# Optimization experiments

Hardware: AMD Instinct MI355X
Metric: run time of the kernel (lower is better)

## Reference

```python
import jax, jax.numpy as jnp
import numpy as np

N = 50000      # nodes
E = 500000     # directed edges
F_IN = 112     # node feature dim
G = 256        # number of graphs in batch


def _lin(key, fan_in, fan_out):
    # torch nn.Linear default init: U(-1/sqrt(fan_in), 1/sqrt(fan_in))
    s = 1.0 / np.sqrt(fan_in)
    kw, kb = jax.random.split(key)
    W = jax.random.uniform(kw, (fan_in, fan_out), jnp.float32, -s, s)
    b = jax.random.uniform(kb, (fan_out,), jnp.float32, -s, s)
    return W, b


def setup_inputs() -> dict:
    key = jax.random.key(0)
    ks = jax.random.split(key, 9)
    x = jax.random.normal(ks[0], (N, F_IN), jnp.float32)
    edge_index = jax.random.randint(ks[1], (2, E), 0, N)
    # sorted graph ids, guaranteeing every graph id 0..G-1 appears
    batch = jnp.sort(jnp.concatenate([jnp.arange(G),
                                      jax.random.randint(ks[2], (N - G,), 0, G)]))
    W1, b1 = _lin(ks[3], F_IN, 336)
    W2, b2 = _lin(ks[4], 336, 168)
    Wg, bg = _lin(ks[5], 168, 84)
    Wf, bf = _lin(ks[6], 84, 42)
    Wo, bo = _lin(ks[7], 42, 1)
    return dict(x=x, edge_index=edge_index, batch=batch,
                W1=W1, b1=b1, W2=W2, b2=b2,
                Wg=Wg, bg=bg, Wf=Wf, bf=bf, Wo=Wo, bo=bo)


def _gcn_conv(x, W, b, src, dst, n):
    """PyG GCNConv: add self-loops, symmetric D^-1/2 A D^-1/2 normalization."""
    h = x @ W                                   # [n, out]
    loop = jnp.arange(n, dtype=src.dtype)
    src_f = jnp.concatenate([src, loop])        # [E+n]
    dst_f = jnp.concatenate([dst, loop])
    deg = jax.ops.segment_sum(jnp.ones(src_f.shape[0], jnp.float32), dst_f, n)
    dinv = jnp.where(deg > 0, jax.lax.rsqrt(deg), 0.0)
    norm = dinv[src_f] * dinv[dst_f]            # [E+n]
    out = jax.ops.segment_sum(h[src_f] * norm[:, None], dst_f, n)
    return out + b


def reference(x, edge_index, batch, W1, b1, W2, b2, Wg, bg, Wf, bf, Wo, bo):
    src, dst = edge_index[0], edge_index[1]
    h = jax.nn.relu(_gcn_conv(x, W1, b1, src, dst, N))
    # dropout is identity in eval mode
    h = jax.nn.relu(_gcn_conv(h, W2, b2, src, dst, N))
    g = jax.ops.segment_max(h, batch, G)        # global max pool -> [G, 168]
    g = jax.nn.relu(g @ Wg + bg)
    g = jax.nn.relu(g @ Wf + bf)
    return g @ Wo + bo                           # [G, 1]
```

## Files before the change

kernel.cpp:

```cpp
#include <hip/hip_runtime.h>
#include <hip/hip_fp16.h>

#define N_NODES 50000
#define MPAD    50048
#define N_EDGES 500000
#define F_IN    112
#define K1X     112
#define K1P     128
#define F1      336
#define K2P     352
#define F2      168
#define NGRAPH  256
#define SCAN_CHUNK 1024
#define SCAN_BLOCKS ((N_NODES + SCAN_CHUNK - 1) / SCAN_CHUNK)

typedef __attribute__((ext_vector_type(8))) _Float16 f16x8;
typedef __attribute__((ext_vector_type(4))) float f32x4;
typedef unsigned short ushort_t;

__device__ __forceinline__ ushort_t f16_bits(float x) {
    __half h = __float2half_rn(x);
    return *(ushort_t*)&h;
}

__device__ __forceinline__ void gload_b64(uint2& d, const ushort_t* a) {
    asm volatile("global_load_dwordx2 %0, %1, off" : "=v"(d) : "v"(a));
}
__device__ __forceinline__ void gload_b128(uint4& d, const ushort_t* a) {
    asm volatile("global_load_dwordx4 %0, %1, off" : "=v"(d) : "v"(a));
}
__device__ __forceinline__ void vmwait0() {
    asm volatile("s_waitcnt vmcnt(0)" ::: "memory");
    __builtin_amdgcn_sched_barrier(0);
}

__global__ void k_zero_int(int* p, int n) {
    int i = blockIdx.x * blockDim.x + threadIdx.x;
    if (i < n) p[i] = 0;
}

#define CVX_ELEMS  (N_NODES * 28)
#define CVX_BLOCKS ((CVX_ELEMS + 255) / 256)
#define CNT_BLOCKS  ((N_EDGES / 2 + 255) / 256)
#define CVW1_BLOCKS ((384 * K1P + 255) / 256)
#define CVW2_BLOCKS ((192 * K2P + 255) / 256)
#define PREP_BLOCKS (CVX_BLOCKS + CNT_BLOCKS + CVW1_BLOCKS + CVW2_BLOCKS)

__global__ __launch_bounds__(256) void k_prep(const float* __restrict__ x,
                                              const int* __restrict__ dst,
                                              const float* __restrict__ W1,
                                              const float* __restrict__ W2,
                                              ushort_t* __restrict__ x16,
                                              int* __restrict__ dcount,
                                              ushort_t* __restrict__ w1t,
                                              ushort_t* __restrict__ w2t) {
    int bid = blockIdx.x;
    int t = threadIdx.x;
    if (bid < CVX_BLOCKS) {
        int i = bid * 256 + t;
        if (i < CVX_ELEMS) {
            float4 f = ((const float4*)x)[i];
            __half2 h0 = __floats2half2_rn(f.x, f.y);
            __half2 h1 = __floats2half2_rn(f.z, f.w);
            uint2 u; u.x = *(unsigned*)&h0; u.y = *(unsigned*)&h1;
            ((uint2*)x16)[i] = u;
        }
        return;
    }
    bid -= CVX_BLOCKS;
    if (bid < CNT_BLOCKS) {
        int i = bid * 256 + t;
        if (i < N_EDGES / 2) {
            int2 d = ((const int2*)dst)[i];
            atomicAdd(&dcount[d.x], 1);
            atomicAdd(&dcount[d.y], 1);
        }
        return;
    }
    bid -= CNT_BLOCKS;
    if (bid < CVW1_BLOCKS) {
        int idx = bid * 256 + t;
        if (idx < 384 * K1P) {
            int n = idx / K1P, k = idx % K1P;
            float v = (n < F1 && k < F_IN) ? W1[k * F1 + n] : 0.0f;
            w1t[idx] = f16_bits(v);
        }
        return;
    }
    bid -= CVW1_BLOCKS;
    {
        int idx = bid * 256 + t;
        if (idx < 192 * K2P) {
            int n = idx / K2P, k = idx % K2P;
            float v = (n < F2 && k < F1) ? W2[k * F2 + n] : 0.0f;
            w2t[idx] = f16_bits(v);
        }
    }
}

__global__ __launch_bounds__(SCAN_CHUNK) void k_scan1(const int* __restrict__ dcount,
                                                      int* __restrict__ off,
                                                      int* __restrict__ partials,
                                                      float* __restrict__ dinv, int n) {
    __shared__ int s[SCAN_CHUNK];
    int t = threadIdx.x;
    int i = blockIdx.x * SCAN_CHUNK + t;
    int val = (i < n) ? dcount[i] : 0;
    s[t] = val;
    __syncthreads();
    for (int d = 1; d < SCAN_CHUNK; d <<= 1) {
        int x = (t >= d) ? s[t - d] : 0;
        __syncthreads();
        s[t] += x;
        __syncthreads();
    }
    if (i < n) {
        off[i] = s[t] - val;
        dinv[i] = rsqrtf((float)val + 1.0f);
    }
    if (t == SCAN_CHUNK - 1) partials[blockIdx.x] = s[t];
}
__global__ __launch_bounds__(SCAN_CHUNK) void k_scan3(int* __restrict__ off,
                                                      const int* __restrict__ partials, int n) {
    __shared__ int tmp[SCAN_BLOCKS];
    __shared__ int pref[SCAN_BLOCKS];
    int t = threadIdx.x;
    if (t < SCAN_BLOCKS) tmp[t] = partials[t];
    __syncthreads();
    if (t == 0) {
        int run = 0;
        for (int j = 0; j < SCAN_BLOCKS; ++j) { pref[j] = run; run += tmp[j]; }
    }
    __syncthreads();
    int i = blockIdx.x * SCAN_CHUNK + t;
    if (i < n) off[i] += pref[blockIdx.x];
    if (i == n) off[i] = N_EDGES;
}

__global__ void k_scatter(const int* __restrict__ src, const int* __restrict__ dst,
                          const int* __restrict__ off, int* __restrict__ cur,
                          const float* __restrict__ dinv,
                          int2* __restrict__ csr, int e2) {
    int i = blockIdx.x * blockDim.x + threadIdx.x;
    if (i >= e2) return;
    int2 s2 = ((const int2*)src)[i];
    int2 d2 = ((const int2*)dst)[i];
    {
        int pos = atomicAdd(&cur[d2.x], 1);
        int2 rec; rec.x = s2.x; rec.y = __float_as_int(dinv[s2.x] * dinv[d2.x]);
        csr[off[d2.x] + pos] = rec;
    }
    {
        int pos = atomicAdd(&cur[d2.y], 1);
        int2 rec; rec.x = s2.y; rec.y = __float_as_int(dinv[s2.y] * dinv[d2.y]);
        csr[off[d2.y] + pos] = rec;
    }
}

__global__ __launch_bounds__(256) void k_agg1(const ushort_t* __restrict__ X16,
                                              const int* __restrict__ off,
                                              const int2* __restrict__ csr,
                                              const float* __restrict__ dinv,
                                              ushort_t* __restrict__ aX) {
    int w = (blockIdx.x * 256 + threadIdx.x) >> 6;
    int lane = threadIdx.x & 63;
    if (w >= N_NODES / 2) return;
    const int g = lane >> 5, sl = lane & 31;
    const int slc = min(sl, 27);
    const int v = 2 * w + g;
    const bool act = sl < 28;
    int o0A = off[2 * w], oM = off[2 * w + 1], o1B = off[2 * w + 2];
    int o0 = g ? oM : o0A;
    int n  = g ? (o1B - oM) : (oM - o0A);
    int nmax = max(oM - o0A, o1B - oM);
    int total = o1B - o0A;
    float di = dinv[v];
    float s2 = di * di;
    float4 acc;
    {
        uint2 us = *(const uint2*)(X16 + (long)v * K1X + slc * 4);
        float2 sf0 = __half22float2(*(__half2*)&us.x);
        float2 sf1 = __half22float2(*(__half2*)&us.y);
        acc.x = sf0.x * s2; acc.y = sf0.y * s2; acc.z = sf1.x * s2; acc.w = sf1.y * s2;
    }
    int nm1 = max(n - 1, 0);
    if (total <= 64) {
        int2 eall = csr[min(o0A + lane, N_EDGES - 1)];
        int ebase = o0 - o0A;
        for (int b = 0; b < nmax; b += 8) {
            int es[8]; float ec[8];
            #pragma unroll
            for (int j = 0; j < 8; ++j) {
                int widx = ebase + min(b + j, nm1);
                es[j] = __shfl(eall.x, widx);
                ec[j] = __int_as_float(__shfl(eall.y, widx));
            }
            uint2 u[8];
            #pragma unroll
            for (int j = 0; j < 8; ++j)
                gload_b64(u[j], X16 + (long)es[j] * K1X + slc * 4);
            vmwait0();
            #pragma unroll
            for (int j = 0; j < 8; ++j) {
                float c = ((b + j) < n) ? ec[j] : 0.0f;
                float2 f0 = __half22float2(*(__half2*)&u[j].x);
                float2 f1 = __half22float2(*(__half2*)&u[j].y);
                acc.x += c * f0.x; acc.y += c * f0.y; acc.z += c * f1.x; acc.w += c * f1.y;
            }
        }
    } else {
        for (int b = 0; b < nmax; b += 8) {
            int2 e[8];
            #pragma unroll
            for (int j = 0; j < 8; ++j) {
                int cidx = min(o0 + min(b + j, nm1), N_EDGES - 1);
                e[j] = csr[cidx];
            }
            uint2 u[8];
            #pragma unroll
            for (int j = 0; j < 8; ++j)
                gload_b64(u[j], X16 + (long)e[j].x * K1X + slc * 4);
            vmwait0();
            #pragma unroll
            for (int j = 0; j < 8; ++j) {
                float c = ((b + j) < n) ? __int_as_float(e[j].y) : 0.0f;
                float2 f0 = __half22float2(*(__half2*)&u[j].x);
                float2 f1 = __half22float2(*(__half2*)&u[j].y);
                acc.x += c * f0.x; acc.y += c * f0.y; acc.z += c * f1.x; acc.w += c * f1.y;
            }
        }
    }
    __half2 h0 = __floats2half2_rn(acc.x, acc.y);
    __half2 h1 = __floats2half2_rn(acc.z, acc.w);
    uint2 o; o.x = *(unsigned*)&h0; o.y = *(unsigned*)&h1;
    if (!act) { o.x = 0; o.y = 0; }
    *(uint2*)(aX + (long)v * K1P + sl * 4) = o;
}

__global__ __launch_bounds__(256) void k_gemm_fused(
        const ushort_t* __restrict__ aX,
        const ushort_t* __restrict__ w1t,
        const float* __restrict__ b1,
        const ushort_t* __restrict__ w2t,
        ushort_t* __restrict__ T2) {
    __shared__ ushort_t As[64][40];
    __shared__ ushort_t Bs[352][40];
    __shared__ ushort_t H1s[64][360];
    const int tid = threadIdx.x;
    const int row0 = blockIdx.x * 64;
    const int w = tid >> 6, l = tid & 63;
    const int wm = w >> 1, wn = w & 1;
    const int lm = l & 15, lq = l >> 4;

    f32x4 acc1[2][11];
    #pragma unroll
    for (int i = 0; i < 2; ++i)
        #pragma unroll
        for (int j = 0; j < 11; ++j) acc1[i][j] = (f32x4){0.f, 0.f, 0.f, 0.f};

    for (int k0 = 0; k0 < K1P; k0 += 32) {
        {
            int r = tid >> 2, s = (tid & 3) * 8;
            *(int4*)&As[r][s] = *(const int4*)&aX[(long)(row0 + r) * K1P + k0 + s];
        }
        #pragma unroll
        for (int it = 0; it < 6; ++it) {
            int f = tid + it * 256;
            if (f < 1408) {
                int r = f >> 2, s = (f & 3) * 8;
                *(int4*)&Bs[r][s] = *(const int4*)&w1t[(long)r * K1P + k0 + s];
            }
        }
        __syncthreads();
        f16x8 af0 = *(const f16x8*)&As[wm * 32 + lm][lq * 8];
        f16x8 af1 = *(const f16x8*)&As[wm * 32 + 16 + lm][lq * 8];
        #pragma unroll
        for (int ns = 0; ns < 11; ++ns) {
            f16x8 bf = *(const f16x8*)&Bs[wn * 176 + ns * 16 + lm][lq * 8];
            acc1[0][ns] = __builtin_amdgcn_mfma_f32_16x16x32_f16(af0, bf, acc1[0][ns], 0, 0, 0);
            acc1[1][ns] = __builtin_amdgcn_mfma_f32_16x16x32_f16(af1, bf, acc1[1][ns], 0, 0, 0);
        }
        __syncthreads();
    }
    #pragma unroll
    for (int ms = 0; ms < 2; ++ms)
        #pragma unroll
        for (int ns = 0; ns < 11; ++ns) {
            int col = wn * 176 + ns * 16 + lm;
            float bb = (col < F1) ? b1[col] : 0.0f;
            #pragma unroll
            for (int i = 0; i < 4; ++i) {
                int r = wm * 32 + ms * 16 + lq * 4 + i;
                H1s[r][col] = f16_bits(fmaxf(acc1[ms][ns][i] + bb, 0.0f));
            }
        }
    __syncthreads();

    f32x4 acc2[2][6];
    #pragma unroll
    for (int i = 0; i < 2; ++i)
        #pragma unroll
        for (int j = 0; j < 6; ++j) acc2[i][j] = (f32x4){0.f, 0.f, 0.f, 0.f};

    for (int k0 = 0; k0 < K2P; k0 += 32) {
        #pragma unroll
        for (int it = 0; it < 3; ++it) {
            int f = tid + it * 256;
            int r = f >> 2, s = (f & 3) * 8;
            *(int4*)&Bs[r][s] = *(const int4*)&w2t[(long)r * K2P + k0 + s];
        }
        __syncthreads();
        f16x8 af0 = *(const f16x8*)&H1s[wm * 32 + lm][k0 + lq * 8];
        f16x8 af1 = *(const f16x8*)&H1s[wm * 32 + 16 + lm][k0 + lq * 8];
        #pragma unroll
        for (int ns = 0; ns < 6; ++ns) {
            f16x8 bf = *(const f16x8*)&Bs[wn * 96 + ns * 16 + lm][lq * 8];
            acc2[0][ns] = __builtin_amdgcn_mfma_f32_16x16x32_f16(af0, bf, acc2[0][ns], 0, 0, 0);
            acc2[1][ns] = __builtin_amdgcn_mfma_f32_16x16x32_f16(af1, bf, acc2[1][ns], 0, 0, 0);
        }
        __syncthreads();
    }
    #pragma unroll
    for (int ms = 0; ms < 2; ++ms)
        #pragma unroll
        for (int ns = 0; ns < 6; ++ns) {
            int col = wn * 96 + ns * 16 + lm;
            if (col < F2) {
                #pragma unroll
                for (int i = 0; i < 4; ++i) {
                    int r = row0 + wm * 32 + ms * 16 + lq * 4 + i;
                    T2[(long)r * F2 + col] = f16_bits(acc2[ms][ns][i]);
                }
            }
        }
}

__global__ __launch_bounds__(256) void k_agg2(const ushort_t* __restrict__ T16,
                                              const int* __restrict__ off,
                                              const int2* __restrict__ csr,
                                              const float* __restrict__ dinv,
                                              const float* __restrict__ b2,
                                              const int* __restrict__ batch,
                                              float* __restrict__ gmax) {
    __shared__ __align__(16) float smax[8][168];
    __shared__ int sb[8];
    int tid = threadIdx.x;
    int w = (blockIdx.x * 256 + tid) >> 6;
    int lane = tid & 63;
    const int g = lane >> 5, sl = lane & 31;
    const int slc = min(sl, 20);
    const int nib = tid >> 5;
    const int v = 2 * w + g;
    const bool act = sl < 21;
    int o0A = off[2 * w], oM = off[2 * w + 1], o1B = off[2 * w + 2];
    int o0 = g ? oM : o0A;
    int n  = g ? (o1B - oM) : (oM - o0A);
    int nmax = max(oM - o0A, o1B - oM);
    int total = o1B - o0A;
    float di = dinv[v];
    float4 a0, a1;
    {
        uint4 u = *(const uint4*)(T16 + (long)v * F2 + slc * 8);
        float2 f0 = __half22float2(*(__half2*)&u.x);
        float2 f1 = __half22float2(*(__half2*)&u.y);
        float2 f2 = __half22float2(*(__half2*)&u.z);
        float2 f3 = __half22float2(*(__half2*)&u.w);
        float s2 = di * di;
        a0.x = f0.x * s2; a0.y = f0.y * s2; a0.z = f1.x * s2; a0.w = f1.y * s2;
        a1.x = f2.x * s2; a1.y = f2.y * s2; a1.z = f3.x * s2; a1.w = f3.y * s2;
    }
    int nm1 = max(n - 1, 0);
    if (total <= 64) {
        int2 eall = csr[min(o0A + lane, N_EDGES - 1)];
        int ebase = o0 - o0A;
        for (int b = 0; b < nmax; b += 8) {
            int es[8]; float ec[8];
            #pragma unroll
            for (int j = 0; j < 8; ++j) {
                int widx = ebase + min(b + j, nm1);
                es[j] = __shfl(eall.x, widx);
                ec[j] = __int_as_float(__shfl(eall.y, widx));
            }
            uint4 u[8];
            #pragma unroll
            for (int j = 0; j < 8; ++j)
                gload_b128(u[j], T16 + (long)es[j] * F2 + slc * 8);
            vmwait0();
            #pragma unroll
            for (int j = 0; j < 8; ++j) {
                float c = ((b + j) < n) ? ec[j] : 0.0f;
                float2 f0 = __half22float2(*(__half2*)&u[j].x);
                float2 f1 = __half22float2(*(__half2*)&u[j].y);
                float2 f2 = __half22float2(*(__half2*)&u[j].z);
                float2 f3 = __half22float2(*(__half2*)&u[j].w);
                a0.x += c * f0.x; a0.y += c * f0.y; a0.z += c * f1.x; a0.w += c * f1.y;
                a1.x += c * f2.x; a1.y += c * f2.y; a1.z += c * f3.x; a1.w += c * f3.y;
            }
        }
    } else {
        for (int b = 0; b < nmax; b += 8) {
            int2 e[8];
            #pragma unroll
            for (int j = 0; j < 8; ++j) {
                int cidx = min(o0 + min(b + j, nm1), N_EDGES - 1);
                e[j] = csr[cidx];
            }
            uint4 u[8];
            #pragma unroll
            for (int j = 0; j < 8; ++j)
                gload_b128(u[j], T16 + (long)e[j].x * F2 + slc * 8);
            vmwait0();
            #pragma unroll
            for (int j = 0; j < 8; ++j) {
                float c = ((b + j) < n) ? __int_as_float(e[j].y) : 0.0f;
                float2 f0 = __half22float2(*(__half2*)&u[j].x);
                float2 f1 = __half22float2(*(__half2*)&u[j].y);
                float2 f2 = __half22float2(*(__half2*)&u[j].z);
                float2 f3 = __half22float2(*(__half2*)&u[j].w);
                a0.x += c * f0.x; a0.y += c * f0.y; a0.z += c * f1.x; a0.w += c * f1.y;
                a1.x += c * f2.x; a1.y += c * f2.y; a1.z += c * f3.x; a1.w += c * f3.y;
            }
        }
    }
    if (act) {
        float4 bb0 = ((const float4*)b2)[sl * 2];
        float4 bb1 = ((const float4*)b2)[sl * 2 + 1];
        a0.x = fmaxf(a0.x + bb0.x, 0.0f); a0.y = fmaxf(a0.y + bb0.y, 0.0f);
        a0.z = fmaxf(a0.z + bb0.z, 0.0f); a0.w = fmaxf(a0.w + bb0.w, 0.0f);
        a1.x = fmaxf(a1.x + bb1.x, 0.0f); a1.y = fmaxf(a1.y + bb1.y, 0.0f);
        a1.z = fmaxf(a1.z + bb1.z, 0.0f); a1.w = fmaxf(a1.w + bb1.w, 0.0f);
        ((float4*)&smax[nib][0])[sl * 2]     = a0;
        ((float4*)&smax[nib][0])[sl * 2 + 1] = a1;
    }
    if ((tid & 31) == 0) sb[nib] = batch[v];
    __syncthreads();
    if (tid < F2) {
        int f = tid;
        int bp = sb[0];
        float m = smax[0][f];
        #pragma unroll
        for (int r = 1; r < 8; ++r) {
            int bc = sb[r];
            float vv = smax[r][f];
            if (bc == bp) { m = fmaxf(m, vv); }
            else {
                atomicMax((int*)&gmax[bp * F2 + f], __float_as_int(m));
                m = vv; bp = bc;
            }
        }
        atomicMax((int*)&gmax[bp * F2 + f], __float_as_int(m));
    }
}

__global__ __launch_bounds__(128) void k_head(const float* __restrict__ gmax,
        const float* __restrict__ Wg, const float* __restrict__ bg,
        const float* __restrict__ Wf, const float* __restrict__ bf,
        const float* __restrict__ Wo, const float* __restrict__ bo,
        float* __restrict__ out) {
    __shared__ float s1[84];
    __shared__ float s2[42];
    int gi = blockIdx.x;
    const float* s0 = gmax + (long)gi * F2;
    int t = threadIdx.x;
    if (t < 84) {
        float acc = bg[t];
        #pragma unroll 4
        for (int k = 0; k < F2; ++k) acc += s0[k] * Wg[k * 84 + t];
        s1[t] = fmaxf(acc, 0.0f);
    }
    __syncthreads();
    if (t < 42) {
        float acc = bf[t];
        #pragma unroll 4
        for (int k = 0; k < 84; ++k) acc += s1[k] * Wf[k * 42 + t];
        s2[t] = fmaxf(acc, 0.0f);
    }
    __syncthreads();
    if (t == 0) {
        float acc = bo[0];
        for (int k = 0; k < 42; ++k) acc += s2[k] * Wo[k];
        out[gi] = acc;
    }
}

extern "C" void kernel_launch(void* const* d_in, const int* in_sizes, int n_in,
                              void* d_out, int out_size, void* d_ws, size_t ws_size,
                              hipStream_t stream) {
    const float* x   = (const float*)d_in[0];
    const int*   ei  = (const int*)d_in[1];
    const int*   bat = (const int*)d_in[2];
    const float* W1  = (const float*)d_in[3];
    const float* b1  = (const float*)d_in[4];
    const float* W2  = (const float*)d_in[5];
    const float* b2  = (const float*)d_in[6];
    const float* Wg  = (const float*)d_in[7];
    const float* bg  = (const float*)d_in[8];
    const float* Wf  = (const float*)d_in[9];
    const float* bf  = (const float*)d_in[10];
    const float* Wo  = (const float*)d_in[11];
    const float* bo  = (const float*)d_in[12];
    float* out = (float*)d_out;

    char* p = (char*)d_ws;
    float* dinv     = (float*)p; p += 50048 * 4;
    int*   dcount   = (int*)p;   p += 50048 * 4;
    int*   cur      = (int*)p;   p += 50048 * 4;
    float* gmax     = (float*)p; p += NGRAPH * F2 * 4;
    int*   off      = (int*)p;   p += 50064 * 4;
    int*   partials = (int*)p;   p += 64 * 4;
    int2*  csr      = (int2*)p;  p += (long)N_EDGES * 8;
    ushort_t* x16   = (ushort_t*)p; p += (long)N_NODES * K1X * 2;
    ushort_t* aX    = (ushort_t*)p; p += (long)MPAD * K1P * 2;
    ushort_t* w1t   = (ushort_t*)p; p += (long)384 * K1P * 2;
    ushort_t* w2t   = (ushort_t*)p; p += (long)192 * K2P * 2;
    ushort_t* t16   = (ushort_t*)p; p += (long)MPAD * F2 * 2;

    const int* src = ei;
    const int* dst = ei + N_EDGES;
    const int B = 256;
    const int ZERO_WORDS = 50048 * 2 + NGRAPH * F2;

    k_zero_int<<<(ZERO_WORDS + B - 1) / B, B, 0, stream>>>(dcount, ZERO_WORDS);
    k_prep<<<PREP_BLOCKS, B, 0, stream>>>(x, dst, W1, W2, x16, dcount, w1t, w2t);
    k_scan1<<<SCAN_BLOCKS, SCAN_CHUNK, 0, stream>>>(dcount, off, partials, dinv, N_NODES);
    k_scan3<<<SCAN_BLOCKS, SCAN_CHUNK, 0, stream>>>(off, partials, N_NODES);
    k_scatter<<<(N_EDGES / 2 + B - 1) / B, B, 0, stream>>>(src, dst, off, cur, dinv, csr, N_EDGES / 2);

    k_agg1<<<(N_NODES / 2 * 64) / 256, 256, 0, stream>>>(x16, off, csr, dinv, aX);
    k_gemm_fused<<<MPAD / 64, 256, 0, stream>>>(aX, w1t, b1, w2t, t16);

    k_agg2<<<(N_NODES / 2 * 64) / 256, 256, 0, stream>>>(t16, off, csr, dinv, b2, bat, gmax);

    k_head<<<NGRAPH, 128, 0, stream>>>(gmax, Wg, bg, Wf, bf, Wo, bo, out);
}
```

Measured before the change: 256.2 us.

## Replace two-pass scan with atomic-based unordered segment offsets per node pair

```diff
diff --git a/kernel.cpp b/kernel.cpp
--- a/kernel.cpp
+++ b/kernel.cpp
@@ -11,8 +11,6 @@
 #define K2P     352
 #define F2      168
 #define NGRAPH  256
-#define SCAN_CHUNK 1024
-#define SCAN_BLOCKS ((N_NODES + SCAN_CHUNK - 1) / SCAN_CHUNK)
 
 typedef __attribute__((ext_vector_type(8))) _Float16 f16x8;
 typedef __attribute__((ext_vector_type(4))) float f32x4;
@@ -98,47 +96,39 @@
     }
 }
 
-__global__ __launch_bounds__(SCAN_CHUNK) void k_scan1(const int* __restrict__ dcount,
-                                                      int* __restrict__ off,
-                                                      int* __restrict__ partials,
-                                                      float* __restrict__ dinv, int n) {
-    __shared__ int s[SCAN_CHUNK];
-    int t = threadIdx.x;
-    int i = blockIdx.x * SCAN_CHUNK + t;
-    int val = (i < n) ? dcount[i] : 0;
-    s[t] = val;
-    __syncthreads();
-    for (int d = 1; d < SCAN_CHUNK; d <<= 1) {
-        int x = (t >= d) ? s[t - d] : 0;
-        __syncthreads();
-        s[t] += x;
-        __syncthreads();
-    }
-    if (i < n) {
-        off[i] = s[t] - val;
-        dinv[i] = rsqrtf((float)val + 1.0f);
-    }
-    if (t == SCAN_CHUNK - 1) partials[blockIdx.x] = s[t];
-}
-__global__ __launch_bounds__(SCAN_CHUNK) void k_scan3(int* __restrict__ off,
-                                                      const int* __restrict__ partials, int n) {
-    __shared__ int tmp[SCAN_BLOCKS];
-    __shared__ int pref[SCAN_BLOCKS];
-    int t = threadIdx.x;
-    if (t < SCAN_BLOCKS) tmp[t] = partials[t];
-    __syncthreads();
-    if (t == 0) {
-        int run = 0;
-        for (int j = 0; j < SCAN_BLOCKS; ++j) { pref[j] = run; run += tmp[j]; }
-    }
-    __syncthreads();
-    int i = blockIdx.x * SCAN_CHUNK + t;
-    if (i < n) off[i] += pref[blockIdx.x];
-    if (i == n) off[i] = N_EDGES;
+__global__ __launch_bounds__(256) void k_offsets(const int* __restrict__ dcount,
+                                                 int* __restrict__ ctr,
+                                                 int* __restrict__ off,
+                                                 int* __restrict__ pend,
+                                                 float* __restrict__ dinv) {
+    int w = blockIdx.x * 256 + threadIdx.x;
+    int lane = threadIdx.x & 63;
+    bool valid = w < N_NODES / 2;
+    int dA = valid ? dcount[2 * w] : 0;
+    int dB = valid ? dcount[2 * w + 1] : 0;
+    int tot = dA + dB;
+    int pre = tot;
+    #pragma unroll
+    for (int d = 1; d < 64; d <<= 1) {
+        int y = __shfl_up(pre, d);
+        if (lane >= d) pre += y;
+    }
+    int wtotal = __shfl(pre, 63);
+    int base = 0;
+    if (lane == 0) base = atomicAdd(ctr, wtotal);
+    base = __shfl(base, 0);
+    int o0 = base + pre - tot;
+    if (valid) {
+        off[2 * w]     = o0;
+        off[2 * w + 1] = o0 + dA;
+        pend[w]        = o0 + tot;
+        dinv[2 * w]     = rsqrtf((float)dA + 1.0f);
+        dinv[2 * w + 1] = rsqrtf((float)dB + 1.0f);
+    }
 }
 
 __global__ void k_scatter(const int* __restrict__ src, const int* __restrict__ dst,
-                          const int* __restrict__ off, int* __restrict__ cur,
+                          const int* __restrict__ off, int* __restrict__ dcount,
                           const float* __restrict__ dinv,
                           int2* __restrict__ csr, int e2) {
     int i = blockIdx.x * blockDim.x + threadIdx.x;
@@ -146,12 +136,12 @@
     int2 s2 = ((const int2*)src)[i];
     int2 d2 = ((const int2*)dst)[i];
     {
-        int pos = atomicAdd(&cur[d2.x], 1);
+        int pos = atomicSub(&dcount[d2.x], 1) - 1;
         int2 rec; rec.x = s2.x; rec.y = __float_as_int(dinv[s2.x] * dinv[d2.x]);
         csr[off[d2.x] + pos] = rec;
     }
     {
-        int pos = atomicAdd(&cur[d2.y], 1);
+        int pos = atomicSub(&dcount[d2.y], 1) - 1;
         int2 rec; rec.x = s2.y; rec.y = __float_as_int(dinv[s2.y] * dinv[d2.y]);
         csr[off[d2.y] + pos] = rec;
     }
@@ -159,6 +149,7 @@
 
 __global__ __launch_bounds__(256) void k_agg1(const ushort_t* __restrict__ X16,
                                               const int* __restrict__ off,
+                                              const int* __restrict__ pend,
                                               const int2* __restrict__ csr,
                                               const float* __restrict__ dinv,
                                               ushort_t* __restrict__ aX) {
@@ -169,7 +160,7 @@
     const int slc = min(sl, 27);
     const int v = 2 * w + g;
     const bool act = sl < 28;
-    int o0A = off[2 * w], oM = off[2 * w + 1], o1B = off[2 * w + 2];
+    int o0A = off[2 * w], oM = off[2 * w + 1], o1B = pend[w];
     int o0 = g ? oM : o0A;
     int n  = g ? (o1B - oM) : (oM - o0A);
     int nmax = max(oM - o0A, o1B - oM);
@@ -337,6 +328,7 @@
 
 __global__ __launch_bounds__(256) void k_agg2(const ushort_t* __restrict__ T16,
                                               const int* __restrict__ off,
+                                              const int* __restrict__ pend,
                                               const int2* __restrict__ csr,
                                               const float* __restrict__ dinv,
                                               const float* __restrict__ b2,
@@ -352,7 +344,7 @@
     const int nib = tid >> 5;
     const int v = 2 * w + g;
     const bool act = sl < 21;
-    int o0A = off[2 * w], oM = off[2 * w + 1], o1B = off[2 * w + 2];
+    int o0A = off[2 * w], oM = off[2 * w + 1], o1B = pend[w];
     int o0 = g ? oM : o0A;
     int n  = g ? (o1B - oM) : (oM - o0A);
     int nmax = max(oM - o0A, o1B - oM);
@@ -504,10 +496,10 @@
     char* p = (char*)d_ws;
     float* dinv     = (float*)p; p += 50048 * 4;
     int*   dcount   = (int*)p;   p += 50048 * 4;
-    int*   cur      = (int*)p;   p += 50048 * 4;
     float* gmax     = (float*)p; p += NGRAPH * F2 * 4;
-    int*   off      = (int*)p;   p += 50064 * 4;
-    int*   partials = (int*)p;   p += 64 * 4;
+    int*   ctr      = (int*)p;   p += 16 * 4;
+    int*   off      = (int*)p;   p += 100096 * 4;
+    int*   pend     = (int*)p;   p += 25024 * 4;
     int2*  csr      = (int2*)p;  p += (long)N_EDGES * 8;
     ushort_t* x16   = (ushort_t*)p; p += (long)N_NODES * K1X * 2;
     ushort_t* aX    = (ushort_t*)p; p += (long)MPAD * K1P * 2;
@@ -518,18 +510,17 @@
     const int* src = ei;
     const int* dst = ei + N_EDGES;
     const int B = 256;
-    const int ZERO_WORDS = 50048 * 2 + NGRAPH * F2;
+    const int ZERO_WORDS = 50048 + NGRAPH * F2 + 16;
 
     k_zero_int<<<(ZERO_WORDS + B - 1) / B, B, 0, stream>>>(dcount, ZERO_WORDS);
     k_prep<<<PREP_BLOCKS, B, 0, stream>>>(x, dst, W1, W2, x16, dcount, w1t, w2t);
-    k_scan1<<<SCAN_BLOCKS, SCAN_CHUNK, 0, stream>>>(dcount, off, partials, dinv, N_NODES);
-    k_scan3<<<SCAN_BLOCKS, SCAN_CHUNK, 0, stream>>>(off, partials, N_NODES);
-    k_scatter<<<(N_EDGES / 2 + B - 1) / B, B, 0, stream>>>(src, dst, off, cur, dinv, csr, N_EDGES / 2);
-
-    k_agg1<<<(N_NODES / 2 * 64) / 256, 256, 0, stream>>>(x16, off, csr, dinv, aX);
+    k_offsets<<<(N_NODES / 2 + B - 1) / B, B, 0, stream>>>(dcount, ctr, off, pend, dinv);
+    k_scatter<<<(N_EDGES / 2 + B - 1) / B, B, 0, stream>>>(src, dst, off, dcount, dinv, csr, N_EDGES / 2);
+
+    k_agg1<<<(N_NODES / 2 * 64) / 256, 256, 0, stream>>>(x16, off, pend, csr, dinv, aX);
     k_gemm_fused<<<MPAD / 64, 256, 0, stream>>>(aX, w1t, b1, w2t, t16);
 
-    k_agg2<<<(N_NODES / 2 * 64) / 256, 256, 0, stream>>>(t16, off, csr, dinv, b2, bat, gmax);
+    k_agg2<<<(N_NODES / 2 * 64) / 256, 256, 0, stream>>>(t16, off, pend, csr, dinv, b2, bat, gmax);
 
     k_head<<<NGRAPH, 128, 0, stream>>>(gmax, Wg, bg, Wf, bf, Wo, bo, out);
 }
```

New measurement: 256.8 us. Within noise of the previous version (+0.3%).
